# Performance work log

Hardware: AMD Instinct MI355X
Metric: run time of the kernel (lower is better)

## Reference

```python
import jax, jax.numpy as jnp
import numpy as np

D_MODEL = 1024
N_HEADS = 16
DEPTH = D_MODEL // N_HEADS  # 64
BATCH, SEQ = 4, 2048


def setup_inputs() -> dict:
    key = jax.random.key(0)
    ks = jax.random.split(key, 8)
    x = jax.random.normal(ks[0], (BATCH, SEQ, D_MODEL), dtype=jnp.float32)
    # Per-head Dense(depth) weights stacked over heads: [H, d_model, depth]
    s = 1.0 / np.sqrt(D_MODEL)
    Wq = jax.random.normal(ks[1], (N_HEADS, D_MODEL, DEPTH), dtype=jnp.float32) * s
    Wk = jax.random.normal(ks[2], (N_HEADS, D_MODEL, DEPTH), dtype=jnp.float32) * s
    Wv = jax.random.normal(ks[3], (N_HEADS, D_MODEL, DEPTH), dtype=jnp.float32) * s
    bq = jnp.zeros((N_HEADS, DEPTH), dtype=jnp.float32)
    bk = jnp.zeros((N_HEADS, DEPTH), dtype=jnp.float32)
    bv = jnp.zeros((N_HEADS, DEPTH), dtype=jnp.float32)
    Wo = jax.random.normal(ks[4], (D_MODEL, D_MODEL), dtype=jnp.float32) * s
    bo = jnp.zeros((D_MODEL,), dtype=jnp.float32)
    return {"x": x, "Wq": Wq, "bq": bq, "Wk": Wk, "bk": bk,
            "Wv": Wv, "bv": bv, "Wo": Wo, "bo": bo}


def reference(x, Wq, bq, Wk, bk, Wv, bv, Wo, bo):
    # Per-head projections, batched over heads: [b, h, s, depth]
    q = jnp.einsum('bsd,hde->bhse', x, Wq) + bq[None, :, None, :]
    k = jnp.einsum('bsd,hde->bhse', x, Wk) + bk[None, :, None, :]
    v = jnp.einsum('bsd,hde->bhse', x, Wv) + bv[None, :, None, :]
    scale = 1.0 / jnp.sqrt(jnp.float32(DEPTH))
    scores = jnp.einsum('bhqe,bhke->bhqk', q, k) * scale  # [b, h, s, s]
    attn = jax.nn.softmax(scores, axis=-1)
    z = jnp.einsum('bhqk,bhke->bhqe', attn, v)  # [b, h, s, depth]
    # Concat heads along last axis (head-major order matches tf.concat of per-head outputs)
    multi_head = z.transpose(0, 2, 1, 3).reshape(BATCH, SEQ, D_MODEL)
    return multi_head @ Wo + bo
```

## Files before the change

kernel.cpp:

```cpp
#include <hip/hip_runtime.h>

typedef unsigned short u16;
typedef __bf16 bf16x8 __attribute__((ext_vector_type(8)));
typedef float f32x4 __attribute__((ext_vector_type(4)));
typedef float f32x16 __attribute__((ext_vector_type(16)));
typedef unsigned int u32x4 __attribute__((ext_vector_type(4)));
typedef unsigned int u32x2 __attribute__((ext_vector_type(2)));

__device__ __forceinline__ u16 f2b(float f) {
  union { float f; unsigned u; } v; v.f = f;
  return (u16)((v.u + 0x7fffu + ((v.u >> 16) & 1u)) >> 16);
}

__device__ __forceinline__ unsigned pkbf(float a, float b) {
#if __has_builtin(__builtin_amdgcn_cvt_pk_bf16_f32)
  typedef __bf16 bf16x2v __attribute__((ext_vector_type(2)));
  bf16x2v r = __builtin_amdgcn_cvt_pk_bf16_f32(a, b);
  return __builtin_bit_cast(unsigned, r);
#else
  return (unsigned)f2b(a) | ((unsigned)f2b(b) << 16);
#endif
}

__device__ __forceinline__ float fexp2(float x) {
#if __has_builtin(__builtin_amdgcn_exp2f)
  return __builtin_amdgcn_exp2f(x);
#else
  return exp2f(x);
#endif
}

__device__ __forceinline__ bf16x8 ldfrag(const u16* p) {
  u32x4 r = *(const u32x4*)p;
  return __builtin_bit_cast(bf16x8, r);
}

#define GLOAD_LDS16(gp, lp)                                                        \
  __builtin_amdgcn_global_load_lds((const __attribute__((address_space(1))) void*)(gp), \
                                   (__attribute__((address_space(3))) void*)(lp), 16, 0, 0)

#define MFMA32(a, b, c) __builtin_amdgcn_mfma_f32_32x32x16_bf16((a), (b), (c), 0, 0, 0)

#define QSC 0.18033688011f


__global__ __launch_bounds__(256) void k_pack(const float* __restrict__ x,
                                              const float* __restrict__ Wq,
                                              const float* __restrict__ Wk,
                                              const float* __restrict__ Wv,
                                              const float* __restrict__ Wo,
                                              u16* __restrict__ xb,
                                              u16* __restrict__ wqkv,
                                              u16* __restrict__ wo_t) {
  const int bid = blockIdx.x, tid = threadIdx.x;
  if (bid < 4096) {
    int i = (bid * 256 + tid) * 8;
    float4 v0 = *(const float4*)(x + i);
    float4 v1 = *(const float4*)(x + i + 4);
    u32x4 o;
    o[0] = pkbf(v0.x, v0.y);
    o[1] = pkbf(v0.z, v0.w);
    o[2] = pkbf(v1.x, v1.y);
    o[3] = pkbf(v1.z, v1.w);
    *(u32x4*)(xb + i) = o;
    return;
  }
  __shared__ u16 tile[64][65];
  if (bid < 4864) {
    int b2 = bid - 4096;
    int p = b2 >> 8, rem = b2 & 255, h = rem >> 4, dt = rem & 15;
    const float* W = (p == 0) ? Wq : (p == 1) ? Wk : Wv;
    for (int i = tid; i < 4096; i += 256) {
      int d = i >> 6, e = i & 63;
      tile[e][d] = f2b(W[h * 65536 + (dt * 64 + d) * 64 + e]);
    }
    __syncthreads();
    for (int i = tid; i < 4096; i += 256) {
      int e = i >> 6, d = i & 63;
      wqkv[(size_t)(p * 1024 + h * 64 + e) * 1024 + dt * 64 + d] = tile[e][d];
    }
  } else {
    int b2 = bid - 4864;
    int kt = b2 >> 4, nt = b2 & 15;
    for (int i = tid; i < 4096; i += 256) {
      int dk = i >> 6, de = i & 63;
      tile[de][dk] = f2b(Wo[(size_t)(kt * 64 + dk) * 1024 + nt * 64 + de]);
    }
    __syncthreads();
    for (int i = tid; i < 4096; i += 256) {
      int de = i >> 6, dk = i & 63;
      wo_t[(size_t)(nt * 64 + de) * 1024 + kt * 64 + dk] = tile[de][dk];
    }
  }
}


template <bool SWAP>
__device__ __forceinline__ void gemm_core32(const u16* __restrict__ A, const u16* __restrict__ Bt,
                                            int row0, int col0, u16* As, u16* Bs, f32x16 acc[2][2]) {
  const int tid = threadIdx.x, w = tid >> 6, lane = tid & 63;
  const int l31 = lane & 31, hi = lane >> 5;
  const int wm = (w >> 1) * 64, wn = (w & 1) * 64;
  for (int k0 = 0; k0 < 1024; k0 += 32) {
#pragma unroll
    for (int i = 0; i < 2; i++) {
      int bse = (w * 2 + i) * 512;
      int flat = bse + lane * 8;
      int r = flat >> 5, c = flat & 31;
      GLOAD_LDS16(A + (size_t)(row0 + r) * 1024 + k0 + c, As + bse);
      GLOAD_LDS16(Bt + (size_t)(col0 + r) * 1024 + k0 + c, Bs + bse);
    }
    __syncthreads();
    bf16x8 af[2][2], bfr[2][2];
#pragma unroll
    for (int t = 0; t < 2; t++)
#pragma unroll
      for (int s = 0; s < 2; s++) {
        af[t][s] = ldfrag(As + (wm + t * 32 + l31) * 32 + s * 16 + hi * 8);
        bfr[t][s] = ldfrag(Bs + (wn + t * 32 + l31) * 32 + s * 16 + hi * 8);
      }
#pragma unroll
    for (int mt = 0; mt < 2; mt++)
#pragma unroll
      for (int nt = 0; nt < 2; nt++)
#pragma unroll
        for (int s = 0; s < 2; s++)
          acc[mt][nt] = SWAP ? MFMA32(bfr[nt][s], af[mt][s], acc[mt][nt])
                             : MFMA32(af[mt][s], bfr[nt][s], acc[mt][nt]);
    __syncthreads();
  }
}


__global__ __launch_bounds__(256) void k_gemm_qkv(const u16* __restrict__ xb, const u16* __restrict__ wt,
                                                  const float* __restrict__ bq, const float* __restrict__ bk,
                                                  const float* __restrict__ bv,
                                                  u16* __restrict__ qo, u16* __restrict__ ko,
                                                  u16* __restrict__ vto) {
  __shared__ u16 As[4096], Bs[4096];
  f32x16 acc[2][2];
#pragma unroll
  for (int a = 0; a < 2; a++)
#pragma unroll
    for (int b = 0; b < 2; b++)
#pragma unroll
      for (int r = 0; r < 16; r++) acc[a][b][r] = 0.f;

  const int row0 = blockIdx.x * 128, col0 = blockIdx.y * 128;
  const int p = blockIdx.y >> 3;
  const int colr = (blockIdx.y & 7) * 128;
  const int tid = threadIdx.x, w = tid >> 6, lane = tid & 63;
  const int l31 = lane & 31, hi = lane >> 5;
  const int wm = (w >> 1) * 64, wn = (w & 1) * 64;

  if (p == 2) {
    gemm_core32<true>(xb, wt, row0, col0, As, Bs, acc);
#pragma unroll
    for (int mt = 0; mt < 2; mt++) {
      int rb = row0 + wm + mt * 32;
      int b_ = rb >> 11;
      int s_ = (rb & 2047) + l31;
#pragma unroll
      for (int nt = 0; nt < 2; nt++) {
        int ebase = colr + wn + nt * 32;
#pragma unroll
        for (int g = 0; g < 4; g++) {
          float4 bvv = *(const float4*)(bv + ebase + g * 8 + hi * 4);
#pragma unroll
          for (int j = 0; j < 4; j++) {
            int rem = ebase + g * 8 + hi * 4 + j;
            int h = rem >> 6, e = rem & 63;
            float val = acc[mt][nt][g * 4 + j] + (&bvv.x)[j];
            vto[(((size_t)(b_ * 16 + h)) * 64 + e) * 2048 + s_] = f2b(val);
          }
        }
      }
    }
  } else {
    gemm_core32<false>(xb, wt, row0, col0, As, Bs, acc);
    u16* dst = (p == 0) ? qo : ko;
    const float* bias = (p == 0) ? bq : bk;
    const float qsc = (p == 0) ? QSC : 1.0f;
#pragma unroll
    for (int nt = 0; nt < 2; nt++) {
      int rem = colr + wn + nt * 32 + l31;
      int h = rem >> 6, e = rem & 63;
      float bval = bias[rem];
#pragma unroll
      for (int mt = 0; mt < 2; mt++) {
        int rb = row0 + wm + mt * 32;
        int b_ = rb >> 11, sb = rb & 2047;
        size_t obase = ((size_t)(b_ * 16 + h) * 2048) * 64 + e;
#pragma unroll
        for (int reg = 0; reg < 16; reg++) {
          int s_ = sb + (reg & 3) + 8 * (reg >> 2) + 4 * hi;
          float val = (acc[mt][nt][reg] + bval) * qsc;
          dst[obase + (size_t)s_ * 64] = f2b(val);
        }
      }
    }
  }
}


__global__ __launch_bounds__(256) void k_gemm_out(const u16* __restrict__ zb, const u16* __restrict__ wt,
                                                  const float* __restrict__ bo, float* __restrict__ out) {
  __shared__ u16 As[4096], Bs[4096];
  f32x16 acc[2][2];
#pragma unroll
  for (int a = 0; a < 2; a++)
#pragma unroll
    for (int b = 0; b < 2; b++)
#pragma unroll
      for (int r = 0; r < 16; r++) acc[a][b][r] = 0.f;

  const int row0 = blockIdx.x * 128, col0 = blockIdx.y * 128;
  gemm_core32<false>(zb, wt, row0, col0, As, Bs, acc);

  const int tid = threadIdx.x, w = tid >> 6, lane = tid & 63;
  const int l31 = lane & 31, hi = lane >> 5;
  const int wm = (w >> 1) * 64, wn = (w & 1) * 64;
#pragma unroll
  for (int nt = 0; nt < 2; nt++) {
    int c = col0 + wn + nt * 32 + l31;
    float bval = bo[c];
#pragma unroll
    for (int mt = 0; mt < 2; mt++) {
      int rb = row0 + wm + mt * 32;
#pragma unroll
      for (int reg = 0; reg < 16; reg++) {
        int r = rb + (reg & 3) + 8 * (reg >> 2) + 4 * hi;
        out[(size_t)r * 1024 + c] = acc[mt][nt][reg] + bval;
      }
    }
  }
}


__global__ __launch_bounds__(256) void k_attn(const u16* __restrict__ q, const u16* __restrict__ k,
                                              const u16* __restrict__ vt, u16* __restrict__ z) {
  __shared__ u16 Ks[64 * 72], Vs[64 * 72], Ps[4][32 * 72];
  const int tid = threadIdx.x, w = tid >> 6, lane = tid & 63;
  const int l31 = lane & 31, hi = lane >> 5;
  const int bh = blockIdx.y, s0 = blockIdx.x * 128;
  const size_t base = (size_t)bh * 2048 * 64;
  const int qrow = s0 + w * 32 + l31;

  bf16x8 qf[4];
  {
    const u16* qp = q + base + (size_t)qrow * 64 + hi * 8;
#pragma unroll
    for (int ks = 0; ks < 4; ks++) qf[ks] = ldfrag(qp + ks * 16);
  }

  f32x16 accT[2], lvec;
#pragma unroll
  for (int r = 0; r < 16; r++) { accT[0][r] = 0.f; accT[1][r] = 0.f; lvec[r] = 0.f; }

  const int srow = tid >> 3;
  const int scol = (tid & 7) * 8;
  const u16* kg = k + base;
  const u16* vg = vt + base;

  u32x4 kr0, kr1, vr0, vr1;
  kr0 = *(const u32x4*)(kg + (size_t)srow * 64 + scol);
  kr1 = *(const u32x4*)(kg + (size_t)(srow + 32) * 64 + scol);
  vr0 = *(const u32x4*)(vg + (size_t)srow * 2048 + scol);
  vr1 = *(const u32x4*)(vg + (size_t)(srow + 32) * 2048 + scol);

  u16* Pw = Ps[w];
  const int poff = l31 * 72;

  for (int kc = 0; kc < 2048; kc += 64) {
    __syncthreads();
    *(u32x4*)&Ks[srow * 72 + scol] = kr0;
    *(u32x4*)&Ks[(srow + 32) * 72 + scol] = kr1;
    *(u32x4*)&Vs[srow * 72 + scol] = vr0;
    *(u32x4*)&Vs[(srow + 32) * 72 + scol] = vr1;
    __syncthreads();
    if (kc + 64 < 2048) {
      int kn = kc + 64;
      kr0 = *(const u32x4*)(kg + (size_t)(kn + srow) * 64 + scol);
      kr1 = *(const u32x4*)(kg + (size_t)(kn + srow + 32) * 64 + scol);
      vr0 = *(const u32x4*)(vg + (size_t)srow * 2048 + kn + scol);
      vr1 = *(const u32x4*)(vg + (size_t)(srow + 32) * 2048 + kn + scol);
    }

    f32x16 sc[2];
#pragma unroll
    for (int t = 0; t < 2; t++) {
#pragma unroll
      for (int r = 0; r < 16; r++) sc[t][r] = 0.f;
#pragma unroll
      for (int ks = 0; ks < 4; ks++) {
        bf16x8 kf = ldfrag(&Ks[(t * 32 + l31) * 72 + ks * 16 + hi * 8]);
        sc[t] = MFMA32(kf, qf[ks], sc[t]);
      }
    }

#pragma unroll
    for (int t = 0; t < 2; t++)
#pragma unroll
      for (int r = 0; r < 16; r++) sc[t][r] = fexp2(sc[t][r]);
    lvec += sc[0];
    lvec += sc[1];

#pragma unroll
    for (int t = 0; t < 2; t++)
#pragma unroll
      for (int r4 = 0; r4 < 4; r4++) {
        u32x2 d;
        d[0] = pkbf(sc[t][r4 * 4 + 0], sc[t][r4 * 4 + 1]);
        d[1] = pkbf(sc[t][r4 * 4 + 2], sc[t][r4 * 4 + 3]);
        *(u32x2*)&Pw[poff + t * 32 + r4 * 8 + hi * 4] = d;
      }

#pragma unroll
    for (int ks = 0; ks < 4; ks++) {
      bf16x8 pf = ldfrag(&Pw[poff + ks * 16 + hi * 8]);
#pragma unroll
      for (int et = 0; et < 2; et++) {
        bf16x8 vf = ldfrag(&Vs[(et * 32 + l31) * 72 + ks * 16 + hi * 8]);
        accT[et] = MFMA32(vf, pf, accT[et]);
      }
    }
  }

  float l = 0.f;
#pragma unroll
  for (int r = 0; r < 16; r++) l += lvec[r];
  l += __shfl_xor(l, 32);
  float inv = 1.f / l;

  const int b_ = bh >> 4, h = bh & 15;
  u16* zr = z + ((size_t)(b_ * 2048 + qrow)) * 1024 + h * 64;
#pragma unroll
  for (int et = 0; et < 2; et++)
#pragma unroll
    for (int rr = 0; rr < 16; rr += 2) {
      unsigned pkd = pkbf(accT[et][rr] * inv, accT[et][rr + 1] * inv);
      int e = et * 32 + (rr & 3) + 8 * (rr >> 2) + 4 * hi;
      *(unsigned*)&zr[e] = pkd;
    }
}


extern "C" void kernel_launch(void* const* d_in, const int* in_sizes, int n_in,
                              void* d_out, int out_size, void* d_ws, size_t ws_size,
                              hipStream_t stream) {
  (void)in_sizes; (void)n_in; (void)out_size;
  const float* x  = (const float*)d_in[0];
  const float* Wq = (const float*)d_in[1];
  const float* bq = (const float*)d_in[2];
  const float* Wk = (const float*)d_in[3];
  const float* bk = (const float*)d_in[4];
  const float* Wv = (const float*)d_in[5];
  const float* bv = (const float*)d_in[6];
  const float* Wo = (const float*)d_in[7];
  const float* bo = (const float*)d_in[8];
  float* out = (float*)d_out;
  char* ws = (char*)d_ws;
  if (ws_size < 92274688u) return;

  u16* xb   = (u16*)(ws + 0);
  u16* wqkv = (u16*)(ws + 16777216);
  u16* wo_t = (u16*)(ws + 23068672);
  u16* qb   = (u16*)(ws + 25165824);
  u16* kb   = (u16*)(ws + 41943040);
  u16* vtb  = (u16*)(ws + 58720256);
  u16* zb   = (u16*)(ws + 75497472);

  k_pack<<<5120, 256, 0, stream>>>(x, Wq, Wk, Wv, Wo, xb, wqkv, wo_t);
  k_gemm_qkv<<<dim3(64, 24), 256, 0, stream>>>(xb, wqkv, bq, bk, bv, qb, kb, vtb);
  k_attn<<<dim3(16, 64), 256, 0, stream>>>(qb, kb, vtb, zb);
  k_gemm_out<<<dim3(64, 8), 256, 0, stream>>>(zb, wo_t, bo, out);
}
```

Baseline: 315.0 us.

## Process two query tiles per wave in attention to reuse K/V fragments

Each wave in the attention kernel now handles 64 query rows (two 32-row sub-tiles) instead of 32, so every block covers 256 queries and the grid is halved. Each K and V fragment loaded from shared memory now feeds two MFMAs, and each staged K/V chunk is reused by twice as many queries, cutting LDS and global traffic per unit of compute. The cost is doubled accumulator and P-buffer storage, which raises register and LDS pressure and puts fewer blocks on the GPU. The fallback bf16 pack path also changes to a round-half-up byte permute, but it only runs when the hardware conversion builtin is missing.

```diff
diff --git a/kernel.cpp b/kernel.cpp
--- a/kernel.cpp
+++ b/kernel.cpp
@@ -18,7 +18,9 @@
   bf16x2v r = __builtin_amdgcn_cvt_pk_bf16_f32(a, b);
   return __builtin_bit_cast(unsigned, r);
 #else
-  return (unsigned)f2b(a) | ((unsigned)f2b(b) << 16);
+  unsigned ua = __builtin_bit_cast(unsigned, a) + 0x8000u;
+  unsigned ub = __builtin_bit_cast(unsigned, b) + 0x8000u;
+  return __builtin_amdgcn_perm(ub, ua, 0x07060302u);
 #endif
 }
 
@@ -237,25 +239,30 @@
 }
 
 
-__global__ __launch_bounds__(256) void k_attn(const u16* __restrict__ q, const u16* __restrict__ k,
-                                              const u16* __restrict__ vt, u16* __restrict__ z) {
-  __shared__ u16 Ks[64 * 72], Vs[64 * 72], Ps[4][32 * 72];
+__global__ __launch_bounds__(256, 2) void k_attn(const u16* __restrict__ q, const u16* __restrict__ k,
+                                                 const u16* __restrict__ vt, u16* __restrict__ z) {
+  __shared__ u16 Ks[64 * 72], Vs[64 * 72], Ps[4][64 * 72];
   const int tid = threadIdx.x, w = tid >> 6, lane = tid & 63;
   const int l31 = lane & 31, hi = lane >> 5;
-  const int bh = blockIdx.y, s0 = blockIdx.x * 128;
+  const int bh = blockIdx.y, s0 = blockIdx.x * 256;
   const size_t base = (size_t)bh * 2048 * 64;
-  const int qrow = s0 + w * 32 + l31;
-
-  bf16x8 qf[4];
-  {
-    const u16* qp = q + base + (size_t)qrow * 64 + hi * 8;
-#pragma unroll
-    for (int ks = 0; ks < 4; ks++) qf[ks] = ldfrag(qp + ks * 16);
-  }
-
-  f32x16 accT[2], lvec;
-#pragma unroll
-  for (int r = 0; r < 16; r++) { accT[0][r] = 0.f; accT[1][r] = 0.f; lvec[r] = 0.f; }
+  const int qrow0 = s0 + w * 64;
+
+  bf16x8 qf[2][4];
+#pragma unroll
+  for (int u = 0; u < 2; u++) {
+    const u16* qp = q + base + (size_t)(qrow0 + u * 32 + l31) * 64 + hi * 8;
+#pragma unroll
+    for (int ks = 0; ks < 4; ks++) qf[u][ks] = ldfrag(qp + ks * 16);
+  }
+
+  f32x16 accT[2][2];
+  f32x16 lvec[2];
+#pragma unroll
+  for (int u = 0; u < 2; u++) {
+#pragma unroll
+    for (int r = 0; r < 16; r++) { accT[u][0][r] = 0.f; accT[u][1][r] = 0.f; lvec[u][r] = 0.f; }
+  }
 
   const int srow = tid >> 3;
   const int scol = (tid & 7) * 8;
@@ -269,7 +276,6 @@
   vr1 = *(const u32x4*)(vg + (size_t)(srow + 32) * 2048 + scol);
 
   u16* Pw = Ps[w];
-  const int poff = l31 * 72;
 
   for (int kc = 0; kc < 2048; kc += 64) {
     __syncthreads();
@@ -286,62 +292,68 @@
       vr1 = *(const u32x4*)(vg + (size_t)(srow + 32) * 2048 + kn + scol);
     }
 
-    f32x16 sc[2];
 #pragma unroll
     for (int t = 0; t < 2; t++) {
-#pragma unroll
-      for (int r = 0; r < 16; r++) sc[t][r] = 0.f;
+      f32x16 scA, scB;
+#pragma unroll
+      for (int r = 0; r < 16; r++) { scA[r] = 0.f; scB[r] = 0.f; }
 #pragma unroll
       for (int ks = 0; ks < 4; ks++) {
         bf16x8 kf = ldfrag(&Ks[(t * 32 + l31) * 72 + ks * 16 + hi * 8]);
-        sc[t] = MFMA32(kf, qf[ks], sc[t]);
-      }
-    }
-
-#pragma unroll
-    for (int t = 0; t < 2; t++)
-#pragma unroll
-      for (int r = 0; r < 16; r++) sc[t][r] = fexp2(sc[t][r]);
-    lvec += sc[0];
-    lvec += sc[1];
-
-#pragma unroll
-    for (int t = 0; t < 2; t++)
+        scA = MFMA32(kf, qf[0][ks], scA);
+        scB = MFMA32(kf, qf[1][ks], scB);
+      }
+#pragma unroll
+      for (int r = 0; r < 16; r++) scA[r] = fexp2(scA[r]);
+      lvec[0] += scA;
+#pragma unroll
+      for (int r = 0; r < 16; r++) scB[r] = fexp2(scB[r]);
+      lvec[1] += scB;
 #pragma unroll
       for (int r4 = 0; r4 < 4; r4++) {
         u32x2 d;
-        d[0] = pkbf(sc[t][r4 * 4 + 0], sc[t][r4 * 4 + 1]);
-        d[1] = pkbf(sc[t][r4 * 4 + 2], sc[t][r4 * 4 + 3]);
-        *(u32x2*)&Pw[poff + t * 32 + r4 * 8 + hi * 4] = d;
-      }
+        d[0] = pkbf(scA[r4 * 4 + 0], scA[r4 * 4 + 1]);
+        d[1] = pkbf(scA[r4 * 4 + 2], scA[r4 * 4 + 3]);
+        *(u32x2*)&Pw[l31 * 72 + t * 32 + r4 * 8 + hi * 4] = d;
+        u32x2 e;
+        e[0] = pkbf(scB[r4 * 4 + 0], scB[r4 * 4 + 1]);
+        e[1] = pkbf(scB[r4 * 4 + 2], scB[r4 * 4 + 3]);
+        *(u32x2*)&Pw[(32 + l31) * 72 + t * 32 + r4 * 8 + hi * 4] = e;
+      }
+    }
 
 #pragma unroll
     for (int ks = 0; ks < 4; ks++) {
-      bf16x8 pf = ldfrag(&Pw[poff + ks * 16 + hi * 8]);
-#pragma unroll
-      for (int et = 0; et < 2; et++) {
-        bf16x8 vf = ldfrag(&Vs[(et * 32 + l31) * 72 + ks * 16 + hi * 8]);
-        accT[et] = MFMA32(vf, pf, accT[et]);
-      }
-    }
-  }
-
-  float l = 0.f;
-#pragma unroll
-  for (int r = 0; r < 16; r++) l += lvec[r];
-  l += __shfl_xor(l, 32);
-  float inv = 1.f / l;
+      bf16x8 vf0 = ldfrag(&Vs[(0 * 32 + l31) * 72 + ks * 16 + hi * 8]);
+      bf16x8 vf1 = ldfrag(&Vs[(1 * 32 + l31) * 72 + ks * 16 + hi * 8]);
+      bf16x8 pf0 = ldfrag(&Pw[l31 * 72 + ks * 16 + hi * 8]);
+      bf16x8 pf1 = ldfrag(&Pw[(32 + l31) * 72 + ks * 16 + hi * 8]);
+      accT[0][0] = MFMA32(vf0, pf0, accT[0][0]);
+      accT[0][1] = MFMA32(vf1, pf0, accT[0][1]);
+      accT[1][0] = MFMA32(vf0, pf1, accT[1][0]);
+      accT[1][1] = MFMA32(vf1, pf1, accT[1][1]);
+    }
+  }
 
   const int b_ = bh >> 4, h = bh & 15;
-  u16* zr = z + ((size_t)(b_ * 2048 + qrow)) * 1024 + h * 64;
-#pragma unroll
-  for (int et = 0; et < 2; et++)
-#pragma unroll
-    for (int rr = 0; rr < 16; rr += 2) {
-      unsigned pkd = pkbf(accT[et][rr] * inv, accT[et][rr + 1] * inv);
-      int e = et * 32 + (rr & 3) + 8 * (rr >> 2) + 4 * hi;
-      *(unsigned*)&zr[e] = pkd;
-    }
+#pragma unroll
+  for (int u = 0; u < 2; u++) {
+    float l = 0.f;
+#pragma unroll
+    for (int r = 0; r < 16; r++) l += lvec[u][r];
+    l += __shfl_xor(l, 32);
+    float inv = 1.f / l;
+    int qrow = qrow0 + u * 32 + l31;
+    u16* zr = z + ((size_t)(b_ * 2048 + qrow)) * 1024 + h * 64;
+#pragma unroll
+    for (int et = 0; et < 2; et++)
+#pragma unroll
+      for (int rr = 0; rr < 16; rr += 2) {
+        unsigned pkd = pkbf(accT[u][et][rr] * inv, accT[u][et][rr + 1] * inv);
+        int e = et * 32 + (rr & 3) + 8 * (rr >> 2) + 4 * hi;
+        *(unsigned*)&zr[e] = pkd;
+      }
+  }
 }
 
 
@@ -372,6 +384,6 @@
 
   k_pack<<<5120, 256, 0, stream>>>(x, Wq, Wk, Wv, Wo, xb, wqkv, wo_t);
   k_gemm_qkv<<<dim3(64, 24), 256, 0, stream>>>(xb, wqkv, bq, bk, bv, qb, kb, vtb);
-  k_attn<<<dim3(16, 64), 256, 0, stream>>>(qb, kb, vtb, zb);
+  k_attn<<<dim3(8, 64), 256, 0, stream>>>(qb, kb, vtb, zb);
   k_gemm_out<<<dim3(64, 8), 256, 0, stream>>>(zb, wo_t, bo, out);
 }
```

Result: faster. 295.6 us (-6.2%).
